# Kernel tuning notes

Measured on AMD Instinct MI355X. Metric: run time of the kernel, lower is better.

Reference implementation:

```python
import jax, jax.numpy as jnp
import numpy as np

# dims: L=tgt len, S=src len, N=batch, E=embed, H=heads
L, S, N, E, H = 1024, 1024, 4, 1024, 16
HD = E // H  # head dim = 64


def setup_inputs() -> dict:
    key = jax.random.key(0)
    ks = jax.random.split(key, 7)
    w_scale = 0.02
    return {
        "query": jax.random.normal(ks[0], (L, N, E), jnp.float32),
        "key": jax.random.normal(ks[1], (S, N, E), jnp.float32),
        "value": jax.random.normal(ks[2], (S, N, E), jnp.float32),
        "in_proj_weight": jax.random.normal(ks[3], (3 * E, E), jnp.float32) * w_scale,
        "in_proj_bias": jax.random.normal(ks[4], (3 * E,), jnp.float32) * w_scale,
        "out_proj_weight": jax.random.normal(ks[5], (E, E), jnp.float32) * w_scale,
        "out_proj_bias": jax.random.normal(ks[6], (E,), jnp.float32) * w_scale,
    }


def reference(query, key, value, in_proj_weight, in_proj_bias,
              out_proj_weight, out_proj_bias):
    scaling = float(HD) ** -0.5
    # packed QKV projection, sliced exactly as the torch code does
    q = (query @ in_proj_weight[:E].T + in_proj_bias[:E]) * scaling        # (L,N,E)
    k = key @ in_proj_weight[E:2 * E].T + in_proj_bias[E:2 * E]            # (S,N,E)
    v = value @ in_proj_weight[2 * E:].T + in_proj_bias[2 * E:]            # (S,N,E)
    # split heads: (L,N,E) -> (N*H, L, HD)
    q = q.reshape(L, N * H, HD).transpose(1, 0, 2)
    k = k.reshape(S, N * H, HD).transpose(1, 0, 2)
    v = v.reshape(S, N * H, HD).transpose(1, 0, 2)
    scores = jnp.einsum('bld,bsd->bls', q, k)          # (N*H, L, S)
    attn = jax.nn.softmax(scores, axis=-1)
    sig = jax.nn.sigmoid(scores)                        # the need_sigmoid_weights variant
    out = jnp.einsum('bls,bsd->bld', attn, v)          # (N*H, L, HD)
    out = out.transpose(1, 0, 2).reshape(L, N, E)
    out = out @ out_proj_weight.T + out_proj_bias       # (L,N,E)
    # weights averaged over heads, as torch MHA returns: (N,L,S)
    attn_weights = attn.reshape(N, H, L, S).sum(axis=1) / H
    sig_weights = sig.reshape(N, H, L, S).sum(axis=1) / H
    return out, attn_weights, sig_weights
```

## Files before the change

### kernel.cpp

```cpp
#include <hip/hip_runtime.h>

#define L_DIM 1024
#define E_DIM 1024
#define NB 4
#define H_NUM 16
#define HD_DIM 64
#define T_TOK 4096
#define NHB 64

typedef float f32x4 __attribute__((ext_vector_type(4)));
typedef unsigned short u16x8 __attribute__((ext_vector_type(8)));
typedef unsigned short u16x4 __attribute__((ext_vector_type(4)));
typedef __bf16 bf16x8 __attribute__((ext_vector_type(8)));

__device__ inline unsigned short f2bf(float f) {
  unsigned int u = __builtin_bit_cast(unsigned int, f);
  u += 0x7FFFu + ((u >> 16) & 1u);
  return (unsigned short)(u >> 16);
}
__device__ inline f32x4 mfma16(u16x8 a, u16x8 b, f32x4 c) {
  return __builtin_amdgcn_mfma_f32_16x16x32_bf16(
      __builtin_bit_cast(bf16x8, a), __builtin_bit_cast(bf16x8, b), c, 0, 0, 0);
}

__device__ __forceinline__ void gl2lds16(const void* g, void* l) {
  auto gp = reinterpret_cast<const __attribute__((address_space(1))) unsigned int*>(
      reinterpret_cast<unsigned long long>(g));
  auto lp = reinterpret_cast<__attribute__((address_space(3))) unsigned int*>(
      static_cast<unsigned int>(reinterpret_cast<unsigned long long>(l)));
  __builtin_amdgcn_global_load_lds(gp, lp, 16, 0, 0);
}

__global__ __launch_bounds__(256) void cast_kernel(
    const float* __restrict__ s0, const float* __restrict__ s1,
    const float* __restrict__ s2, const float* __restrict__ s3,
    unsigned short* __restrict__ d0, unsigned short* __restrict__ d1,
    unsigned short* __restrict__ d2, unsigned short* __restrict__ d3,
    int n0, int n1, int n2, int n3) {
  const int y = blockIdx.y;
  const float* s = (y == 0) ? s0 : (y == 1) ? s1 : (y == 2) ? s2 : s3;
  unsigned short* d = (y == 0) ? d0 : (y == 1) ? d1 : (y == 2) ? d2 : d3;
  const int n = (y == 0) ? n0 : (y == 1) ? n1 : (y == 2) ? n2 : n3;
  int idx = (blockIdx.x * 256 + threadIdx.x) * 8;
  const int stride = gridDim.x * 256 * 8;
  for (; idx < n; idx += stride) {
    float4 a = *(const float4*)(s + idx);
    float4 b = *(const float4*)(s + idx + 4);
    u16x8 o = {f2bf(a.x), f2bf(a.y), f2bf(a.z), f2bf(a.w),
               f2bf(b.x), f2bf(b.y), f2bf(b.z), f2bf(b.w)};
    *(u16x8*)(d + idx) = o;
  }
}

__device__ __forceinline__ void stage_tile(const unsigned short* __restrict__ g,
                                           unsigned short* lbuf, int tid) {
  const int r = tid >> 2, c = tid & 3;
  const int sc = c ^ ((r ^ (r >> 2)) & 3);
  gl2lds16(g + (size_t)r * 1024 + sc * 8, lbuf + tid * 8);
  const int r2 = r + 64;
  gl2lds16(g + (size_t)r2 * 1024 + sc * 8, lbuf + (tid + 256) * 8);
}
__device__ __forceinline__ int frag_off(int r, int q) {
  return r * 32 + ((q ^ ((r ^ (r >> 2)) & 3)) << 3);
}

__global__ __launch_bounds__(256) void qkv_gemm(
    const unsigned short* __restrict__ qb, const unsigned short* __restrict__ kb,
    const unsigned short* __restrict__ vb, const unsigned short* __restrict__ Wb,
    const float* __restrict__ bias, unsigned short* __restrict__ q_hm,
    unsigned short* __restrict__ k_hm, unsigned short* __restrict__ v_t) {
  __shared__ __align__(16) unsigned short As[2][4096];
  __shared__ __align__(16) unsigned short Bs[2][4096];
  const int tid = threadIdx.x;
  const int bm = blockIdx.x, bn = blockIdx.y, z = blockIdx.z;
  const unsigned short* Ag = ((z == 0) ? qb : (z == 1) ? kb : vb) + (size_t)bm * 128 * 1024;
  const unsigned short* Bg = Wb + (size_t)z * 1048576 + (size_t)bn * 128 * 1024;
  const float* bc = bias + z * E_DIM;

  const int w = tid >> 6, lane = tid & 63;
  const int wm = w & 1, wn = w >> 1;
  const int quad = lane >> 4, l16 = lane & 15;

  f32x4 acc[4][4];
#pragma unroll
  for (int i = 0; i < 4; i++)
#pragma unroll
    for (int j = 0; j < 4; j++) { f32x4 zz = {0.f, 0.f, 0.f, 0.f}; acc[i][j] = zz; }

  stage_tile(Ag, As[0], tid);
  stage_tile(Bg, Bs[0], tid);

  for (int kk = 0; kk < 32; kk++) {
    __syncthreads();
    if (kk + 1 < 32) {
      const int bf = (kk + 1) & 1;
      stage_tile(Ag + (kk + 1) * 32, As[bf], tid);
      stage_tile(Bg + (kk + 1) * 32, Bs[bf], tid);
    }
    const int cb = kk & 1;
    u16x8 af[4], bfv[4];
#pragma unroll
    for (int mi = 0; mi < 4; mi++) {
      int r = wm * 64 + mi * 16 + l16;
      af[mi] = *(const u16x8*)&As[cb][frag_off(r, quad)];
    }
#pragma unroll
    for (int ni = 0; ni < 4; ni++) {
      int r = wn * 64 + ni * 16 + l16;
      bfv[ni] = *(const u16x8*)&Bs[cb][frag_off(r, quad)];
    }
#pragma unroll
    for (int mi = 0; mi < 4; mi++)
#pragma unroll
      for (int ni = 0; ni < 4; ni++)
        acc[mi][ni] = mfma16(af[mi], bfv[ni], acc[mi][ni]);
  }
#pragma unroll
  for (int ni = 0; ni < 4; ni++) {
    int col = bn * 128 + wn * 64 + ni * 16 + l16;
    float bv = bc[col];
    int h = col >> 6, d = col & 63;
#pragma unroll
    for (int mi = 0; mi < 4; mi++) {
#pragma unroll
      for (int r = 0; r < 4; r++) {
        int t = bm * 128 + wm * 64 + mi * 16 + quad * 4 + r;
        float v = acc[mi][ni][r] + bv;
        int nb = t & 3, pos = t >> 2;
        if (z == 0) {
          v *= 0.125f;
          q_hm[(size_t)((nb * 16 + h) * 1024 + pos) * 64 + d] = f2bf(v);
        } else if (z == 1) {
          k_hm[(size_t)((nb * 16 + h) * 1024 + pos) * 64 + d] = f2bf(v);
        } else {
          v_t[(size_t)((nb * 16 + h) * 64 + d) * 1024 + pos] = f2bf(v);
        }
      }
    }
  }
}

__global__ __launch_bounds__(256, 2) void attn_kernel(
    const unsigned short* __restrict__ q_hm, const unsigned short* __restrict__ k_hm,
    const unsigned short* __restrict__ v_t, unsigned short* __restrict__ o_h,
    float* __restrict__ m_ws, float* __restrict__ r_ws) {
  __shared__ __align__(16) unsigned short stage[2][4096];
  __shared__ __align__(16) unsigned short pt[2][32][68];
  __shared__ float red_m[4][32];
  __shared__ float red_s[4][32];

  const int tid = threadIdx.x;
  const int l0 = blockIdx.x * 32;
  const int b = blockIdx.y;
  const int nb = b >> 4, h = b & 15;
  const int w = tid >> 6, lane = tid & 63;
  const int quad = lane >> 4, l16 = lane & 15;

  const int i1 = tid + 256;
  const int r0s = tid >> 3, c0s = tid & 7;
  const int r1s = i1 >> 3, c1s = i1 & 7;
  const int src0 = (c0s ^ (r0s & 7)) * 8;
  const int src1 = (c1s ^ (r1s & 7)) * 8;

  const unsigned short* kbase = k_hm + ((size_t)b << 16);
  const unsigned short* vbase = v_t + ((size_t)b << 16);

  u16x8 bq[2][2];
#pragma unroll
  for (int g = 0; g < 2; g++) {
    const unsigned short* qp =
        q_hm + ((size_t)(b * 1024 + l0 + g * 16 + l16) << 6) + quad * 8;
    bq[g][0] = *(const u16x8*)qp;
    bq[g][1] = *(const u16x8*)(qp + 32);
  }

  f32x4 acc[16][2];
#pragma unroll
  for (int j = 0; j < 16; j++)
#pragma unroll
    for (int g = 0; g < 2; g++) { f32x4 z = {0.f, 0.f, 0.f, 0.f}; acc[j][g] = z; }

  gl2lds16(kbase + ((size_t)r0s << 6) + src0, &stage[0][tid * 8]);
  gl2lds16(kbase + ((size_t)r1s << 6) + src1, &stage[0][i1 * 8]);

  const int myrow = w * 16 + l16;
  const int sw0 = ((quad ^ (l16 & 7)) * 8);
  const int sw1 = (((quad + 4) ^ (l16 & 7)) * 8);

#pragma unroll
  for (int j = 0; j < 16; j++) {
    __syncthreads();
    if (j < 15) {
      int bf = (j + 1) & 1;
      gl2lds16(kbase + ((size_t)((j + 1) * 64 + r0s) << 6) + src0, &stage[bf][tid * 8]);
      gl2lds16(kbase + ((size_t)((j + 1) * 64 + r1s) << 6) + src1, &stage[bf][i1 * 8]);
    } else {
      gl2lds16(vbase + ((size_t)r0s << 10) + src0, &stage[0][tid * 8]);
      gl2lds16(vbase + ((size_t)r1s << 10) + src1, &stage[0][i1 * 8]);
    }
    const unsigned short* kt = &stage[j & 1][myrow * 64];
    u16x8 ak0 = *(const u16x8*)(kt + sw0);
    u16x8 ak1 = *(const u16x8*)(kt + sw1);
    acc[j][0] = mfma16(ak0, bq[0][0], acc[j][0]);
    acc[j][0] = mfma16(ak1, bq[0][1], acc[j][0]);
    acc[j][1] = mfma16(ak0, bq[1][0], acc[j][1]);
    acc[j][1] = mfma16(ak1, bq[1][1], acc[j][1]);
  }

  float lm0 = -3e38f, lm1 = -3e38f;
#pragma unroll
  for (int j = 0; j < 16; j++)
#pragma unroll
    for (int r = 0; r < 4; r++) {
      lm0 = fmaxf(lm0, acc[j][0][r]);
      lm1 = fmaxf(lm1, acc[j][1][r]);
    }
  lm0 = fmaxf(lm0, __shfl_xor(lm0, 16, 64));
  lm0 = fmaxf(lm0, __shfl_xor(lm0, 32, 64));
  lm1 = fmaxf(lm1, __shfl_xor(lm1, 16, 64));
  lm1 = fmaxf(lm1, __shfl_xor(lm1, 32, 64));
  if (lane < 16) { red_m[w][lane] = lm0; red_m[w][lane + 16] = lm1; }
  __syncthreads();
  float m0 = fmaxf(fmaxf(red_m[0][l16], red_m[1][l16]),
                   fmaxf(red_m[2][l16], red_m[3][l16]));
  float m1 = fmaxf(fmaxf(red_m[0][l16 + 16], red_m[1][l16 + 16]),
                   fmaxf(red_m[2][l16 + 16], red_m[3][l16 + 16]));

  float ls0 = 0.f, ls1 = 0.f;
#pragma unroll
  for (int j = 0; j < 16; j++) {
#pragma unroll
    for (int r = 0; r < 4; r++) {
      float e0 = __expf(acc[j][0][r] - m0);
      float e1 = __expf(acc[j][1][r] - m1);
      acc[j][0][r] = e0;
      acc[j][1][r] = e1;
      ls0 += e0;
      ls1 += e1;
    }
  }
  ls0 += __shfl_xor(ls0, 16, 64);
  ls0 += __shfl_xor(ls0, 32, 64);
  ls1 += __shfl_xor(ls1, 16, 64);
  ls1 += __shfl_xor(ls1, 32, 64);
  if (lane < 16) { red_s[w][lane] = ls0; red_s[w][lane + 16] = ls1; }
  __syncthreads();
  float rv0 = 1.0f / (red_s[0][l16] + red_s[1][l16] + red_s[2][l16] + red_s[3][l16]);
  float rv1 = 1.0f / (red_s[0][l16 + 16] + red_s[1][l16 + 16] +
                      red_s[2][l16 + 16] + red_s[3][l16 + 16]);
  if (tid < 32) {
    float mm = fmaxf(fmaxf(red_m[0][tid], red_m[1][tid]),
                     fmaxf(red_m[2][tid], red_m[3][tid]));
    float ss = red_s[0][tid] + red_s[1][tid] + red_s[2][tid] + red_s[3][tid];
    m_ws[b * 1024 + l0 + tid] = mm;
    r_ws[b * 1024 + l0 + tid] = 1.0f / ss;
  }

  {
    u16x4 p0 = {f2bf(acc[0][0][0]), f2bf(acc[0][0][1]), f2bf(acc[0][0][2]), f2bf(acc[0][0][3])};
    u16x4 p1 = {f2bf(acc[0][1][0]), f2bf(acc[0][1][1]), f2bf(acc[0][1][2]), f2bf(acc[0][1][3])};
    *(u16x4*)&pt[0][l16][w * 16 + quad * 4] = p0;
    *(u16x4*)&pt[0][16 + l16][w * 16 + quad * 4] = p1;
  }

  f32x4 oacc0 = {0.f, 0.f, 0.f, 0.f};
  f32x4 oacc1 = {0.f, 0.f, 0.f, 0.f};
#pragma unroll
  for (int j = 0; j < 16; j++) {
    __syncthreads();
    if (j < 15) {
      int bf = (j + 1) & 1;
      gl2lds16(vbase + ((size_t)r0s << 10) + (j + 1) * 64 + src0, &stage[bf][tid * 8]);
      gl2lds16(vbase + ((size_t)r1s << 10) + (j + 1) * 64 + src1, &stage[bf][i1 * 8]);
      u16x4 p0 = {f2bf(acc[j + 1][0][0]), f2bf(acc[j + 1][0][1]),
                  f2bf(acc[j + 1][0][2]), f2bf(acc[j + 1][0][3])};
      u16x4 p1 = {f2bf(acc[j + 1][1][0]), f2bf(acc[j + 1][1][1]),
                  f2bf(acc[j + 1][1][2]), f2bf(acc[j + 1][1][3])};
      *(u16x4*)&pt[bf][l16][w * 16 + quad * 4] = p0;
      *(u16x4*)&pt[bf][16 + l16][w * 16 + quad * 4] = p1;
    }
    const unsigned short* vt = &stage[j & 1][myrow * 64];
    u16x8 bv0 = *(const u16x8*)(vt + sw0);
    u16x8 bv1 = *(const u16x8*)(vt + sw1);
    u16x8 ap00 = *(const u16x8*)&pt[j & 1][l16][quad * 8];
    u16x8 ap01 = *(const u16x8*)&pt[j & 1][l16][32 + quad * 8];
    u16x8 ap10 = *(const u16x8*)&pt[j & 1][16 + l16][quad * 8];
    u16x8 ap11 = *(const u16x8*)&pt[j & 1][16 + l16][32 + quad * 8];
    oacc0 = mfma16(ap00, bv0, oacc0);
    oacc0 = mfma16(ap01, bv1, oacc0);
    oacc1 = mfma16(ap10, bv0, oacc1);
    oacc1 = mfma16(ap11, bv1, oacc1);
  }

#pragma unroll
  for (int r = 0; r < 4; r++) {
    int lr = quad * 4 + r;
    float rr0 = __shfl(rv0, lr, 64);
    float rr1 = __shfl(rv1, lr, 64);
    int t0 = (l0 + lr) * 4 + nb;
    int t1 = (l0 + 16 + lr) * 4 + nb;
    o_h[((size_t)t0 << 10) + h * 64 + w * 16 + l16] = f2bf(oacc0[r] * rr0);
    o_h[((size_t)t1 << 10) + h * 64 + w * 16 + l16] = f2bf(oacc1[r] * rr1);
  }
}

__global__ __launch_bounds__(256) void weights_kernel(
    const unsigned short* __restrict__ q_hm, const unsigned short* __restrict__ k_hm,
    const float* __restrict__ m_ws, const float* __restrict__ r_ws,
    float* __restrict__ attn_out, float* __restrict__ sig_out) {
  __shared__ __align__(16) unsigned short qs[2][4096];
  __shared__ __align__(16) unsigned short ks[2][4096];
  __shared__ float ml[16][64];
  __shared__ float rl[16][64];
  __shared__ float cl[16][64];

  const int tid = threadIdx.x;
  const int s0 = blockIdx.x * 64;
  const int l0 = blockIdx.y * 64;
  const int nb = blockIdx.z;
  const int w = tid >> 6, lane = tid & 63;
  const int quad = lane >> 4, l16 = lane & 15;

  const int i1 = tid + 256;
  const int r0s = tid >> 3, c0s = tid & 7;
  const int r1s = i1 >> 3, c1s = i1 & 7;
  const int src0 = (c0s ^ (r0s & 7)) * 8;
  const int src1 = (c1s ^ (r1s & 7)) * 8;

  {
    int idx = tid * 4;
    int hh = idx >> 6, ii = idx & 63;
    int bb = nb * 16 + hh;
    float4 mv4 = *(const float4*)&m_ws[bb * 1024 + l0 + ii];
    float4 rv4 = *(const float4*)&r_ws[bb * 1024 + l0 + ii];
    *(float4*)&ml[hh][ii] = mv4;
    *(float4*)&rl[hh][ii] = rv4;
    float4 cv4 = {__expf(-mv4.x), __expf(-mv4.y), __expf(-mv4.z), __expf(-mv4.w)};
    *(float4*)&cl[hh][ii] = cv4;
  }

  {
    int bb = nb * 16;
    const unsigned short* qb = q_hm + ((size_t)(bb * 1024 + l0) << 6);
    const unsigned short* kb = k_hm + ((size_t)(bb * 1024 + s0) << 6);
    gl2lds16(qb + (r0s << 6) + src0, &qs[0][tid * 8]);
    gl2lds16(qb + (r1s << 6) + src1, &qs[0][i1 * 8]);
    gl2lds16(kb + (r0s << 6) + src0, &ks[0][tid * 8]);
    gl2lds16(kb + (r1s << 6) + src1, &ks[0][i1 * 8]);
  }

  const int sw0 = ((quad ^ (l16 & 7)) * 8);
  const int sw1 = (((quad + 4) ^ (l16 & 7)) * 8);

  f32x4 accA[4], accS[4];
#pragma unroll
  for (int i = 0; i < 4; i++) {
    f32x4 zz = {0.f, 0.f, 0.f, 0.f};
    accA[i] = zz; accS[i] = zz;
  }

#pragma unroll
  for (int h = 0; h < 16; h++) {
    __syncthreads();
    if (h + 1 < 16) {
      int bf = (h + 1) & 1;
      int bb = nb * 16 + h + 1;
      const unsigned short* qb = q_hm + ((size_t)(bb * 1024 + l0) << 6);
      const unsigned short* kb = k_hm + ((size_t)(bb * 1024 + s0) << 6);
      gl2lds16(qb + (r0s << 6) + src0, &qs[bf][tid * 8]);
      gl2lds16(qb + (r1s << 6) + src1, &qs[bf][i1 * 8]);
      gl2lds16(kb + (r0s << 6) + src0, &ks[bf][tid * 8]);
      gl2lds16(kb + (r1s << 6) + src1, &ks[bf][i1 * 8]);
    }
    const int bf = h & 1;
    const unsigned short* qt = &qs[bf][(w * 16 + l16) * 64];
    u16x8 a0 = *(const u16x8*)(qt + sw0);
    u16x8 a1 = *(const u16x8*)(qt + sw1);
    f32x4 mv = *(const f32x4*)&ml[h][w * 16 + quad * 4];
    f32x4 rv = *(const f32x4*)&rl[h][w * 16 + quad * 4];
    f32x4 cv = *(const f32x4*)&cl[h][w * 16 + quad * 4];
#pragma unroll
    for (int ni = 0; ni < 4; ni++) {
      const unsigned short* kt = &ks[bf][(ni * 16 + l16) * 64];
      u16x8 b0 = *(const u16x8*)(kt + sw0);
      u16x8 b1 = *(const u16x8*)(kt + sw1);
      f32x4 scv = {0.f, 0.f, 0.f, 0.f};
      scv = mfma16(a0, b0, scv);
      scv = mfma16(a1, b1, scv);
#pragma unroll
      for (int r = 0; r < 4; r++) {
        float e = __expf(scv[r] - mv[r]);
        accA[ni][r] += e * rv[r];
        accS[ni][r] += e * __builtin_amdgcn_rcpf(e + cv[r]);
      }
    }
  }
  const float inv_h = 1.0f / 16.0f;
  const int lrow0 = l0 + w * 16;
#pragma unroll
  for (int ni = 0; ni < 4; ni++) {
#pragma unroll
    for (int r = 0; r < 4; r++) {
      int l = lrow0 + quad * 4 + r;
      int s = s0 + ni * 16 + l16;
      size_t idx = ((size_t)nb * 1024 + l) * 1024 + s;
      attn_out[idx] = accA[ni][r] * inv_h;
      sig_out[idx] = accS[ni][r] * inv_h;
    }
  }
}

__global__ __launch_bounds__(256) void out_gemm(
    const unsigned short* __restrict__ o_h, const unsigned short* __restrict__ Wb,
    const float* __restrict__ bias, float* __restrict__ out) {
  __shared__ __align__(16) unsigned short As[2][4096];
  __shared__ __align__(16) unsigned short Bs[2][4096];
  const int tid = threadIdx.x;
  const int bm = blockIdx.x, bn = blockIdx.y;
  const unsigned short* Ag = o_h + (size_t)bm * 128 * 1024;
  const unsigned short* Bg = Wb + (size_t)bn * 128 * 1024;

  const int w = tid >> 6, lane = tid & 63;
  const int wm = w & 1, wn = w >> 1;
  const int quad = lane >> 4, l16 = lane & 15;

  f32x4 acc[4][4];
#pragma unroll
  for (int i = 0; i < 4; i++)
#pragma unroll
    for (int j = 0; j < 4; j++) { f32x4 zz = {0.f, 0.f, 0.f, 0.f}; acc[i][j] = zz; }

  stage_tile(Ag, As[0], tid);
  stage_tile(Bg, Bs[0], tid);

  for (int kk = 0; kk < 32; kk++) {
    __syncthreads();
    if (kk + 1 < 32) {
      const int bf = (kk + 1) & 1;
      stage_tile(Ag + (kk + 1) * 32, As[bf], tid);
      stage_tile(Bg + (kk + 1) * 32, Bs[bf], tid);
    }
    const int cb = kk & 1;
    u16x8 af[4], bfv[4];
#pragma unroll
    for (int mi = 0; mi < 4; mi++) {
      int r = wm * 64 + mi * 16 + l16;
      af[mi] = *(const u16x8*)&As[cb][frag_off(r, quad)];
    }
#pragma unroll
    for (int ni = 0; ni < 4; ni++) {
      int r = wn * 64 + ni * 16 + l16;
      bfv[ni] = *(const u16x8*)&Bs[cb][frag_off(r, quad)];
    }
#pragma unroll
    for (int mi = 0; mi < 4; mi++)
#pragma unroll
      for (int ni = 0; ni < 4; ni++)
        acc[mi][ni] = mfma16(af[mi], bfv[ni], acc[mi][ni]);
  }
#pragma unroll
  for (int ni = 0; ni < 4; ni++) {
    int col = bn * 128 + wn * 64 + ni * 16 + l16;
    float bv = bias[col];
#pragma unroll
    for (int mi = 0; mi < 4; mi++) {
#pragma unroll
      for (int r = 0; r < 4; r++) {
        int t = bm * 128 + wm * 64 + mi * 16 + quad * 4 + r;
        out[(size_t)t * E_DIM + col] = acc[mi][ni][r] + bv;
      }
    }
  }
}

extern "C" void kernel_launch(void* const* d_in, const int* in_sizes, int n_in,
                              void* d_out, int out_size, void* d_ws, size_t ws_size,
                              hipStream_t stream) {
  const float* qin  = (const float*)d_in[0];
  const float* kin  = (const float*)d_in[1];
  const float* vin  = (const float*)d_in[2];
  const float* Wqkv = (const float*)d_in[3];
  const float* bqkv = (const float*)d_in[4];
  const float* Wout = (const float*)d_in[5];
  const float* bout = (const float*)d_in[6];
  float* out      = (float*)d_out;
  float* attn_out = out + 4194304;
  float* sig_out  = out + 8388608;

  unsigned short* q_hm = (unsigned short*)d_ws;
  unsigned short* k_hm = q_hm + 4194304;
  unsigned short* v_t  = q_hm + 8388608;
  unsigned short* o_h  = q_hm + 12582912;
  float* m_ws = (float*)(q_hm + 16777216);
  float* r_ws = m_ws + 65536;

  unsigned short* qb = (unsigned short*)(out + 4194304);
  unsigned short* kb = qb + 4194304;
  unsigned short* vb = qb + 8388608;
  unsigned short* Wqkvb = o_h;
  unsigned short* Woutb = v_t;

  cast_kernel<<<dim3(2048, 4), 256, 0, stream>>>(
      qin, kin, vin, Wqkv, qb, kb, vb, Wqkvb,
      4194304, 4194304, 4194304, 3145728);
  qkv_gemm<<<dim3(32, 8, 3), 256, 0, stream>>>(qb, kb, vb, Wqkvb, bqkv,
                                               q_hm, k_hm, v_t);
  attn_kernel<<<dim3(32, 64), 256, 0, stream>>>(q_hm, k_hm, v_t, o_h, m_ws, r_ws);
  cast_kernel<<<dim3(512, 1), 256, 0, stream>>>(
      Wout, Wout, Wout, Wout, Woutb, Woutb, Woutb, Woutb,
      1048576, 0, 0, 0);
  weights_kernel<<<dim3(16, 16, 4), 256, 0, stream>>>(q_hm, k_hm, m_ws, r_ws,
                                                      attn_out, sig_out);
  out_gemm<<<dim3(32, 8), 256, 0, stream>>>(o_h, Woutb, bout, out);
}
```

Measured before the change: 290.6 us.

## Deepen attention K/V prefetch to an 8-slot ring with manual waitcnt barriers

Expands the LDS staging buffer from 2 to 8 slots and prefetches K/V tiles three steps ahead, replacing __syncthreads with explicit vmcnt/lgkmcnt waits plus s_barrier so global loads stay in flight across iterations. It also remaps block indices so neighbouring blocks spread across heads, and defers the m/r workspace stores until after the PV loop. The aim is to hide global-load latency behind the MFMA work. In exchange, the kernel uses about 64KB of LDS, which may reduce the 2-blocks-per-CU occupancy, and the hand-written waitcnt counts must exactly match the number of outstanding loads.

```diff
diff --git a/kernel.cpp b/kernel.cpp
--- a/kernel.cpp
+++ b/kernel.cpp
@@ -144,14 +144,16 @@
     const unsigned short* __restrict__ q_hm, const unsigned short* __restrict__ k_hm,
     const unsigned short* __restrict__ v_t, unsigned short* __restrict__ o_h,
     float* __restrict__ m_ws, float* __restrict__ r_ws) {
-  __shared__ __align__(16) unsigned short stage[2][4096];
+  __shared__ __align__(16) unsigned short stage[8][4096];
   __shared__ __align__(16) unsigned short pt[2][32][68];
   __shared__ float red_m[4][32];
   __shared__ float red_s[4][32];
 
   const int tid = threadIdx.x;
-  const int l0 = blockIdx.x * 32;
-  const int b = blockIdx.y;
+  const int flat = blockIdx.x + (blockIdx.y << 5);
+  const int nf = (flat & 7) * 256 + (flat >> 3);
+  const int l0 = (nf & 31) * 32;
+  const int b = nf >> 5;
   const int nb = b >> 4, h = b & 15;
   const int w = tid >> 6, lane = tid & 63;
   const int quad = lane >> 4, l16 = lane & 15;
@@ -173,6 +175,7 @@
     bq[g][0] = *(const u16x8*)qp;
     bq[g][1] = *(const u16x8*)(qp + 32);
   }
+  asm volatile("" ::: "memory");
 
   f32x4 acc[16][2];
 #pragma unroll
@@ -180,8 +183,11 @@
 #pragma unroll
     for (int g = 0; g < 2; g++) { f32x4 z = {0.f, 0.f, 0.f, 0.f}; acc[j][g] = z; }
 
-  gl2lds16(kbase + ((size_t)r0s << 6) + src0, &stage[0][tid * 8]);
-  gl2lds16(kbase + ((size_t)r1s << 6) + src1, &stage[0][i1 * 8]);
+#pragma unroll
+  for (int t = 0; t < 3; t++) {
+    gl2lds16(kbase + ((size_t)(t * 64 + r0s) << 6) + src0, &stage[t][tid * 8]);
+    gl2lds16(kbase + ((size_t)(t * 64 + r1s) << 6) + src1, &stage[t][i1 * 8]);
+  }
 
   const int myrow = w * 16 + l16;
   const int sw0 = ((quad ^ (l16 & 7)) * 8);
@@ -189,16 +195,22 @@
 
 #pragma unroll
   for (int j = 0; j < 16; j++) {
-    __syncthreads();
-    if (j < 15) {
-      int bf = (j + 1) & 1;
-      gl2lds16(kbase + ((size_t)((j + 1) * 64 + r0s) << 6) + src0, &stage[bf][tid * 8]);
-      gl2lds16(kbase + ((size_t)((j + 1) * 64 + r1s) << 6) + src1, &stage[bf][i1 * 8]);
+    if (j + 3 < 16) {
+      gl2lds16(kbase + ((size_t)((j + 3) * 64 + r0s) << 6) + src0,
+               &stage[(j + 3) & 7][tid * 8]);
+      gl2lds16(kbase + ((size_t)((j + 3) * 64 + r1s) << 6) + src1,
+               &stage[(j + 3) & 7][i1 * 8]);
     } else {
-      gl2lds16(vbase + ((size_t)r0s << 10) + src0, &stage[0][tid * 8]);
-      gl2lds16(vbase + ((size_t)r1s << 10) + src1, &stage[0][i1 * 8]);
-    }
-    const unsigned short* kt = &stage[j & 1][myrow * 64];
+      const int vt = j + 3 - 16;
+      gl2lds16(vbase + ((size_t)r0s << 10) + vt * 64 + src0,
+               &stage[(j + 3) & 7][tid * 8]);
+      gl2lds16(vbase + ((size_t)r1s << 10) + vt * 64 + src1,
+               &stage[(j + 3) & 7][i1 * 8]);
+    }
+    asm volatile("s_waitcnt vmcnt(6)" ::: "memory");
+    __builtin_amdgcn_s_barrier();
+    asm volatile("" ::: "memory");
+    const unsigned short* kt = &stage[j & 7][myrow * 64];
     u16x8 ak0 = *(const u16x8*)(kt + sw0);
     u16x8 ak1 = *(const u16x8*)(kt + sw1);
     acc[j][0] = mfma16(ak0, bq[0][0], acc[j][0]);
@@ -220,11 +232,17 @@
   lm1 = fmaxf(lm1, __shfl_xor(lm1, 16, 64));
   lm1 = fmaxf(lm1, __shfl_xor(lm1, 32, 64));
   if (lane < 16) { red_m[w][lane] = lm0; red_m[w][lane + 16] = lm1; }
-  __syncthreads();
+  asm volatile("s_waitcnt lgkmcnt(0)" ::: "memory");
+  __builtin_amdgcn_s_barrier();
+  asm volatile("" ::: "memory");
   float m0 = fmaxf(fmaxf(red_m[0][l16], red_m[1][l16]),
                    fmaxf(red_m[2][l16], red_m[3][l16]));
   float m1 = fmaxf(fmaxf(red_m[0][l16 + 16], red_m[1][l16 + 16]),
                    fmaxf(red_m[2][l16 + 16], red_m[3][l16 + 16]));
+  float mm = 0.f;
+  if (tid < 32)
+    mm = fmaxf(fmaxf(red_m[0][tid], red_m[1][tid]),
+               fmaxf(red_m[2][tid], red_m[3][tid]));
 
   float ls0 = 0.f, ls1 = 0.f;
 #pragma unroll
@@ -244,17 +262,15 @@
   ls1 += __shfl_xor(ls1, 16, 64);
   ls1 += __shfl_xor(ls1, 32, 64);
   if (lane < 16) { red_s[w][lane] = ls0; red_s[w][lane + 16] = ls1; }
-  __syncthreads();
+  asm volatile("s_waitcnt lgkmcnt(0)" ::: "memory");
+  __builtin_amdgcn_s_barrier();
+  asm volatile("" ::: "memory");
   float rv0 = 1.0f / (red_s[0][l16] + red_s[1][l16] + red_s[2][l16] + red_s[3][l16]);
   float rv1 = 1.0f / (red_s[0][l16 + 16] + red_s[1][l16 + 16] +
                       red_s[2][l16 + 16] + red_s[3][l16 + 16]);
-  if (tid < 32) {
-    float mm = fmaxf(fmaxf(red_m[0][tid], red_m[1][tid]),
-                     fmaxf(red_m[2][tid], red_m[3][tid]));
-    float ss = red_s[0][tid] + red_s[1][tid] + red_s[2][tid] + red_s[3][tid];
-    m_ws[b * 1024 + l0 + tid] = mm;
-    r_ws[b * 1024 + l0 + tid] = 1.0f / ss;
-  }
+  float ssv = 1.f;
+  if (tid < 32)
+    ssv = red_s[0][tid] + red_s[1][tid] + red_s[2][tid] + red_s[3][tid];
 
   {
     u16x4 p0 = {f2bf(acc[0][0][0]), f2bf(acc[0][0][1]), f2bf(acc[0][0][2]), f2bf(acc[0][0][3])};
@@ -267,11 +283,22 @@
   f32x4 oacc1 = {0.f, 0.f, 0.f, 0.f};
 #pragma unroll
   for (int j = 0; j < 16; j++) {
-    __syncthreads();
+    if (j < 13) {
+      const int t = j + 3;
+      gl2lds16(vbase + ((size_t)r0s << 10) + t * 64 + src0, &stage[t & 7][tid * 8]);
+      gl2lds16(vbase + ((size_t)r1s << 10) + t * 64 + src1, &stage[t & 7][i1 * 8]);
+      asm volatile("s_waitcnt vmcnt(6) lgkmcnt(0)" ::: "memory");
+    } else if (j == 13) {
+      asm volatile("s_waitcnt vmcnt(4) lgkmcnt(0)" ::: "memory");
+    } else if (j == 14) {
+      asm volatile("s_waitcnt vmcnt(2) lgkmcnt(0)" ::: "memory");
+    } else {
+      asm volatile("s_waitcnt vmcnt(0) lgkmcnt(0)" ::: "memory");
+    }
+    __builtin_amdgcn_s_barrier();
+    asm volatile("" ::: "memory");
     if (j < 15) {
-      int bf = (j + 1) & 1;
-      gl2lds16(vbase + ((size_t)r0s << 10) + (j + 1) * 64 + src0, &stage[bf][tid * 8]);
-      gl2lds16(vbase + ((size_t)r1s << 10) + (j + 1) * 64 + src1, &stage[bf][i1 * 8]);
+      const int bf = (j + 1) & 1;
       u16x4 p0 = {f2bf(acc[j + 1][0][0]), f2bf(acc[j + 1][0][1]),
                   f2bf(acc[j + 1][0][2]), f2bf(acc[j + 1][0][3])};
       u16x4 p1 = {f2bf(acc[j + 1][1][0]), f2bf(acc[j + 1][1][1]),
@@ -279,7 +306,7 @@
       *(u16x4*)&pt[bf][l16][w * 16 + quad * 4] = p0;
       *(u16x4*)&pt[bf][16 + l16][w * 16 + quad * 4] = p1;
     }
-    const unsigned short* vt = &stage[j & 1][myrow * 64];
+    const unsigned short* vt = &stage[j & 7][myrow * 64];
     u16x8 bv0 = *(const u16x8*)(vt + sw0);
     u16x8 bv1 = *(const u16x8*)(vt + sw1);
     u16x8 ap00 = *(const u16x8*)&pt[j & 1][l16][quad * 8];
@@ -290,6 +317,11 @@
     oacc0 = mfma16(ap01, bv1, oacc0);
     oacc1 = mfma16(ap10, bv0, oacc1);
     oacc1 = mfma16(ap11, bv1, oacc1);
+  }
+
+  if (tid < 32) {
+    m_ws[b * 1024 + l0 + tid] = mm;
+    r_ws[b * 1024 + l0 + tid] = 1.0f / ssv;
   }
 
 #pragma unroll
```

Result: faster. 276.3 us (-4.9%).
